# Kernel optimization log

Measured on AMD Instinct MI355X. Metric: run time of the kernel, lower is better.

## Reference

```python
import jax, jax.numpy as jnp
import numpy as np

V, H, E, L = 50257, 2048, 1024, 4


def setup_inputs() -> dict:
    key = jax.random.key(0)
    ks = jax.random.split(key, 9)
    s = 0.02
    emb = jax.random.normal(ks[0], (V, E), dtype=jnp.float32) * s
    W_ih0 = jax.random.normal(ks[1], (4 * H, E), dtype=jnp.float32) * s   # layer 0 input weights
    W_ihR = jax.random.normal(ks[2], (L - 1, 4 * H, H), dtype=jnp.float32) * s  # layers 1..L-1
    W_hh = jax.random.normal(ks[3], (L, 4 * H, H), dtype=jnp.float32) * s
    b_ih = jax.random.normal(ks[4], (L, 4 * H), dtype=jnp.float32) * s
    b_hh = jax.random.normal(ks[5], (L, 4 * H), dtype=jnp.float32) * s
    fc_W = jax.random.normal(ks[6], (E, H), dtype=jnp.float32) * s
    fc_b = jax.random.normal(ks[7], (E,), dtype=jnp.float32) * s
    inp = jax.random.randint(ks[8], (1,), 0, V, dtype=jnp.int64 if jax.config.jax_enable_x64 else jnp.int32)
    hidden = jnp.zeros((L, 1, H), dtype=jnp.float32)
    cell = jnp.zeros((L, 1, H), dtype=jnp.float32)
    return {"input": inp, "hidden": hidden, "cell": cell, "emb": emb,
            "W_ih0": W_ih0, "W_ihR": W_ihR, "W_hh": W_hh, "b_ih": b_ih,
            "b_hh": b_hh, "fc_W": fc_W, "fc_b": fc_b}


def reference(input, hidden, cell, emb, W_ih0, W_ihR, W_hh, b_ih, b_hh, fc_W, fc_b):
    # embedding lookup: [1, E]
    x = emb[input]
    h_out, c_out = [], []
    for l in range(L):  # small fixed layer loop (structurally distinct weights)
        W_ih = W_ih0 if l == 0 else W_ihR[l - 1]
        gates = x @ W_ih.T + hidden[l] @ W_hh[l].T + b_ih[l] + b_hh[l]  # [1, 4H]
        i, f, g, o = jnp.split(gates, 4, axis=-1)  # torch gate order i,f,g,o
        i, f, o = jax.nn.sigmoid(i), jax.nn.sigmoid(f), jax.nn.sigmoid(o)
        g = jnp.tanh(g)
        c = f * cell[l] + i * g
        h = o * jnp.tanh(c)
        h_out.append(h)
        c_out.append(c)
        x = h
    hidden_new = jnp.stack(h_out, axis=0)  # [L, 1, H]
    cell_new = jnp.stack(c_out, axis=0)
    decoded = x @ fc_W.T + fc_b  # [1, E]
    return decoded, hidden_new, cell_new
```

## Files before the change

kernel.cpp:

```cpp
#include <hip/hip_runtime.h>
#include <math.h>

#define LSTM_H 2048
#define LSTM_E 1024
#define LSTM_L 4

__device__ __forceinline__ float sigmoidf_(float x) {
    return 1.0f / (1.0f + __expf(-x));
}

template<int INW>
__global__ __launch_bounds__(256)
void lstm_layer_kernel(const float* __restrict__ W_ih,
                       const float* __restrict__ W_hh,
                       const float* __restrict__ b_ih,
                       const float* __restrict__ b_hh,
                       const float* __restrict__ xbase,
                       const int*   __restrict__ token,
                       const float* __restrict__ h_in,
                       const float* __restrict__ c_in,
                       float* __restrict__ h_out,
                       float* __restrict__ c_out)
{
    const int j    = blockIdx.x;
    const int wave = threadIdx.x >> 6;
    const int lane = threadIdx.x & 63;

    const float* x = xbase;
    if (token) x += (size_t)(*token) * (size_t)INW;

    const int row = wave * LSTM_H + j;

    const float4* __restrict__ wih4 = (const float4*)(W_ih + (size_t)row * INW);
    const float4* __restrict__ whh4 = (const float4*)(W_hh + (size_t)row * LSTM_H);
    const float4* __restrict__ x4   = (const float4*)x;
    const float4* __restrict__ h4   = (const float4*)h_in;

    float s = 0.0f;

    constexpr int NI = (INW / 4) / 64;
    #pragma unroll
    for (int t = 0; t < NI; ++t) {
        const int idx = lane + t * 64;
        float4 w = wih4[idx];
        float4 v = x4[idx];
        s += w.x * v.x + w.y * v.y + w.z * v.z + w.w * v.w;
    }

    constexpr int NH = (LSTM_H / 4) / 64;
    #pragma unroll
    for (int t = 0; t < NH; ++t) {
        const int idx = lane + t * 64;
        float4 w = whh4[idx];
        float4 v = h4[idx];
        s += w.x * v.x + w.y * v.y + w.z * v.z + w.w * v.w;
    }

    #pragma unroll
    for (int off = 32; off > 0; off >>= 1)
        s += __shfl_down(s, off, 64);

    __shared__ float gsh[4];
    if (lane == 0)
        gsh[wave] = s + b_ih[row] + b_hh[row];
    __syncthreads();

    if (threadIdx.x == 0) {
        const float gi = gsh[0];
        const float gf = gsh[1];
        const float gg = gsh[2];
        const float go = gsh[3];
        const float i_ = sigmoidf_(gi);
        const float f_ = sigmoidf_(gf);
        const float g_ = tanhf(gg);
        const float o_ = sigmoidf_(go);
        const float c  = f_ * c_in[j] + i_ * g_;
        const float h  = o_ * tanhf(c);
        c_out[j] = c;
        h_out[j] = h;
    }
}

__global__ __launch_bounds__(256)
void fc_kernel(const float* __restrict__ fc_W,
               const float* __restrict__ fc_b,
               const float* __restrict__ h,
               float* __restrict__ out)
{
    const int wave = threadIdx.x >> 6;
    const int lane = threadIdx.x & 63;
    const int r = blockIdx.x * 4 + wave;

    const float4* __restrict__ w4 = (const float4*)(fc_W + (size_t)r * LSTM_H);
    const float4* __restrict__ h4 = (const float4*)h;

    float s = 0.0f;
    constexpr int NH = (LSTM_H / 4) / 64;
    #pragma unroll
    for (int t = 0; t < NH; ++t) {
        const int idx = lane + t * 64;
        float4 w = w4[idx];
        float4 v = h4[idx];
        s += w.x * v.x + w.y * v.y + w.z * v.z + w.w * v.w;
    }

    #pragma unroll
    for (int off = 32; off > 0; off >>= 1)
        s += __shfl_down(s, off, 64);

    if (lane == 0)
        out[r] = s + fc_b[r];
}

extern "C" void kernel_launch(void* const* d_in, const int* in_sizes, int n_in,
                              void* d_out, int out_size, void* d_ws, size_t ws_size,
                              hipStream_t stream) {
    const int*   token  = (const int*)d_in[0];
    const float* hidden = (const float*)d_in[1];
    const float* cell   = (const float*)d_in[2];
    const float* emb    = (const float*)d_in[3];
    const float* W_ih0  = (const float*)d_in[4];
    const float* W_ihR  = (const float*)d_in[5];
    const float* W_hh   = (const float*)d_in[6];
    const float* b_ih   = (const float*)d_in[7];
    const float* b_hh   = (const float*)d_in[8];
    const float* fc_W   = (const float*)d_in[9];
    const float* fc_b   = (const float*)d_in[10];

    float* out     = (float*)d_out;
    float* decoded = out;
    float* h_new   = out + LSTM_E;
    float* c_new   = out + LSTM_E + LSTM_L * LSTM_H;

    const size_t WIH_STRIDE = (size_t)4 * LSTM_H * LSTM_H;
    const size_t B_STRIDE   = (size_t)4 * LSTM_H;

    lstm_layer_kernel<LSTM_E><<<LSTM_H, 256, 0, stream>>>(
        W_ih0, W_hh, b_ih, b_hh,
        emb, token,
        hidden, cell,
        h_new, c_new);

    for (int l = 1; l < LSTM_L; ++l) {
        lstm_layer_kernel<LSTM_H><<<LSTM_H, 256, 0, stream>>>(
            W_ihR + (size_t)(l - 1) * WIH_STRIDE,
            W_hh  + (size_t)l * WIH_STRIDE,
            b_ih  + (size_t)l * B_STRIDE,
            b_hh  + (size_t)l * B_STRIDE,
            h_new + (size_t)(l - 1) * LSTM_H, nullptr,
            hidden + (size_t)l * LSTM_H,
            cell   + (size_t)l * LSTM_H,
            h_new + (size_t)l * LSTM_H,
            c_new + (size_t)l * LSTM_H);
    }

    fc_kernel<<<LSTM_E / 4, 256, 0, stream>>>(
        fc_W, fc_b, h_new + (size_t)(LSTM_L - 1) * LSTM_H, decoded);
}
```

Before: 106.9 us.

## Fuse LSTM layers and FC into one cooperative kernel with early W_hh work

Replaces the five separate launches with one persistent cooperative kernel that uses grid-wide syncs between layers. The recurrent W_hh products for layers 1-3 depend only on the input hidden state, so they are computed up front and stored in workspace. This moves about half of the weight traffic off the serial layer-to-layer chain and removes launch gaps. The costs are grid.sync overhead, fewer resident blocks looping over rows, and reliance on the cooperative launch succeeding, with the old multi-kernel path kept as a fallback.

```diff
diff --git a/kernel.cpp b/kernel.cpp
--- a/kernel.cpp
+++ b/kernel.cpp
@@ -1,12 +1,151 @@
 #include <hip/hip_runtime.h>
+#include <hip/hip_cooperative_groups.h>
 #include <math.h>
 
 #define LSTM_H 2048
 #define LSTM_E 1024
 #define LSTM_L 4
 
+namespace cg = cooperative_groups;
+
 __device__ __forceinline__ float sigmoidf_(float x) {
     return 1.0f / (1.0f + __expf(-x));
+}
+
+__device__ __forceinline__ float wave_reduce(float s) {
+    #pragma unroll
+    for (int off = 32; off > 0; off >>= 1)
+        s += __shfl_down(s, off, 64);
+    return s;
+}
+
+__device__ __forceinline__ float dot2048(const float* __restrict__ w,
+                                         const float* __restrict__ v, int lane) {
+    const float4* __restrict__ w4 = (const float4*)w;
+    const float4* __restrict__ v4 = (const float4*)v;
+    float s = 0.0f;
+    #pragma unroll
+    for (int t = 0; t < 8; ++t) {
+        const int idx = lane + t * 64;
+        float4 a = w4[idx];
+        float4 b = v4[idx];
+        s += a.x * b.x + a.y * b.y + a.z * b.z + a.w * b.w;
+    }
+    return s;
+}
+
+__device__ __forceinline__ float dot1024(const float* __restrict__ w,
+                                         const float* __restrict__ v, int lane) {
+    const float4* __restrict__ w4 = (const float4*)w;
+    const float4* __restrict__ v4 = (const float4*)v;
+    float s = 0.0f;
+    #pragma unroll
+    for (int t = 0; t < 4; ++t) {
+        const int idx = lane + t * 64;
+        float4 a = w4[idx];
+        float4 b = v4[idx];
+        s += a.x * b.x + a.y * b.y + a.z * b.z + a.w * b.w;
+    }
+    return s;
+}
+
+__global__ __launch_bounds__(256, 4)
+void lstm_fused_kernel(const int*   __restrict__ token,
+                       const float* __restrict__ hidden,
+                       const float* __restrict__ cell,
+                       const float* __restrict__ emb,
+                       const float* __restrict__ W_ih0,
+                       const float* __restrict__ W_ihR,
+                       const float* __restrict__ W_hh,
+                       const float* __restrict__ b_ih,
+                       const float* __restrict__ b_hh,
+                       const float* __restrict__ fc_W,
+                       const float* __restrict__ fc_b,
+                       float*       __restrict__ out,
+                       float*       __restrict__ part)
+{
+    cg::grid_group grid = cg::this_grid();
+
+    const int G    = gridDim.x;
+    const int b    = blockIdx.x;
+    const int wave = threadIdx.x >> 6;
+    const int lane = threadIdx.x & 63;
+
+    float* decoded = out;
+    float* h_new   = out + LSTM_E;
+    float* c_new   = out + LSTM_E + LSTM_L * LSTM_H;
+
+    __shared__ float gsh[4];
+
+    const float* xemb = emb + (size_t)(*token) * LSTM_E;
+
+    for (int j = b; j < LSTM_H; j += G) {
+        const int row = wave * LSTM_H + j;
+        float s = dot1024(W_ih0 + (size_t)row * LSTM_E, xemb, lane)
+                + dot2048(W_hh  + (size_t)row * LSTM_H, hidden, lane);
+        s = wave_reduce(s);
+        if (lane == 0) gsh[wave] = s + b_ih[row] + b_hh[row];
+        __syncthreads();
+        if (threadIdx.x == 0) {
+            const float i_ = sigmoidf_(gsh[0]);
+            const float f_ = sigmoidf_(gsh[1]);
+            const float g_ = tanhf(gsh[2]);
+            const float o_ = sigmoidf_(gsh[3]);
+            const float c  = f_ * cell[j] + i_ * g_;
+            c_new[j] = c;
+            h_new[j] = o_ * tanhf(c);
+        }
+        __syncthreads();
+    }
+
+    #pragma unroll
+    for (int l = 1; l < LSTM_L; ++l) {
+        const float* hl = hidden + (size_t)l * LSTM_H;
+        for (int j = b; j < LSTM_H; j += G) {
+            const int row = wave * LSTM_H + j;
+            const size_t w_off = (size_t)l * 4 * LSTM_H * LSTM_H + (size_t)row * LSTM_H;
+            float s = dot2048(W_hh + w_off, hl, lane);
+            s = wave_reduce(s);
+            if (lane == 0)
+                part[(size_t)(l - 1) * 4 * LSTM_H + row] =
+                    s + b_ih[(size_t)l * 4 * LSTM_H + row]
+                      + b_hh[(size_t)l * 4 * LSTM_H + row];
+        }
+    }
+
+    grid.sync();
+
+    for (int l = 1; l < LSTM_L; ++l) {
+        const float* hx = h_new + (size_t)(l - 1) * LSTM_H;
+        for (int j = b; j < LSTM_H; j += G) {
+            const int row = wave * LSTM_H + j;
+            float s = dot2048(W_ihR + (size_t)(l - 1) * 4 * LSTM_H * LSTM_H
+                                    + (size_t)row * LSTM_H, hx, lane);
+            s = wave_reduce(s);
+            if (lane == 0) gsh[wave] = s + part[(size_t)(l - 1) * 4 * LSTM_H + row];
+            __syncthreads();
+            if (threadIdx.x == 0) {
+                const float i_ = sigmoidf_(gsh[0]);
+                const float f_ = sigmoidf_(gsh[1]);
+                const float g_ = tanhf(gsh[2]);
+                const float o_ = sigmoidf_(gsh[3]);
+                const float c  = f_ * cell[(size_t)l * LSTM_H + j] + i_ * g_;
+                c_new[(size_t)l * LSTM_H + j] = c;
+                h_new[(size_t)l * LSTM_H + j] = o_ * tanhf(c);
+            }
+            __syncthreads();
+        }
+        grid.sync();
+    }
+
+    {
+        const float* h3 = h_new + (size_t)(LSTM_L - 1) * LSTM_H;
+        for (int r = b * 4 + wave; r < LSTM_E; r += G * 4) {
+            float s = dot2048(fc_W + (size_t)r * LSTM_H, h3, lane);
+            s = wave_reduce(s);
+            if (lane == 0) decoded[r] = s + fc_b[r];
+        }
+    }
 }
 
 template<int INW>
@@ -31,53 +170,26 @@
 
     const int row = wave * LSTM_H + j;
 
-    const float4* __restrict__ wih4 = (const float4*)(W_ih + (size_t)row * INW);
-    const float4* __restrict__ whh4 = (const float4*)(W_hh + (size_t)row * LSTM_H);
-    const float4* __restrict__ x4   = (const float4*)x;
-    const float4* __restrict__ h4   = (const float4*)h_in;
-
     float s = 0.0f;
-
-    constexpr int NI = (INW / 4) / 64;
-    #pragma unroll
-    for (int t = 0; t < NI; ++t) {
-        const int idx = lane + t * 64;
-        float4 w = wih4[idx];
-        float4 v = x4[idx];
-        s += w.x * v.x + w.y * v.y + w.z * v.z + w.w * v.w;
-    }
-
-    constexpr int NH = (LSTM_H / 4) / 64;
-    #pragma unroll
-    for (int t = 0; t < NH; ++t) {
-        const int idx = lane + t * 64;
-        float4 w = whh4[idx];
-        float4 v = h4[idx];
-        s += w.x * v.x + w.y * v.y + w.z * v.z + w.w * v.w;
-    }
-
-    #pragma unroll
-    for (int off = 32; off > 0; off >>= 1)
-        s += __shfl_down(s, off, 64);
+    if (INW == LSTM_E)
+        s += dot1024(W_ih + (size_t)row * INW, x, lane);
+    else
+        s += dot2048(W_ih + (size_t)row * INW, x, lane);
+    s += dot2048(W_hh + (size_t)row * LSTM_H, h_in, lane);
+    s = wave_reduce(s);
 
     __shared__ float gsh[4];
-    if (lane == 0)
-        gsh[wave] = s + b_ih[row] + b_hh[row];
+    if (lane == 0) gsh[wave] = s + b_ih[row] + b_hh[row];
     __syncthreads();
 
     if (threadIdx.x == 0) {
-        const float gi = gsh[0];
-        const float gf = gsh[1];
-        const float gg = gsh[2];
-        const float go = gsh[3];
-        const float i_ = sigmoidf_(gi);
-        const float f_ = sigmoidf_(gf);
-        const float g_ = tanhf(gg);
-        const float o_ = sigmoidf_(go);
+        const float i_ = sigmoidf_(gsh[0]);
+        const float f_ = sigmoidf_(gsh[1]);
+        const float g_ = tanhf(gsh[2]);
+        const float o_ = sigmoidf_(gsh[3]);
         const float c  = f_ * c_in[j] + i_ * g_;
-        const float h  = o_ * tanhf(c);
         c_out[j] = c;
-        h_out[j] = h;
+        h_out[j] = o_ * tanhf(c);
     }
 }
 
@@ -91,25 +203,9 @@
     const int lane = threadIdx.x & 63;
     const int r = blockIdx.x * 4 + wave;
 
-    const float4* __restrict__ w4 = (const float4*)(fc_W + (size_t)r * LSTM_H);
-    const float4* __restrict__ h4 = (const float4*)h;
-
-    float s = 0.0f;
-    constexpr int NH = (LSTM_H / 4) / 64;
-    #pragma unroll
-    for (int t = 0; t < NH; ++t) {
-        const int idx = lane + t * 64;
-        float4 w = w4[idx];
-        float4 v = h4[idx];
-        s += w.x * v.x + w.y * v.y + w.z * v.z + w.w * v.w;
-    }
-
-    #pragma unroll
-    for (int off = 32; off > 0; off >>= 1)
-        s += __shfl_down(s, off, 64);
-
-    if (lane == 0)
-        out[r] = s + fc_b[r];
+    float s = dot2048(fc_W + (size_t)r * LSTM_H, h, lane);
+    s = wave_reduce(s);
+    if (lane == 0) out[r] = s + fc_b[r];
 }
 
 extern "C" void kernel_launch(void* const* d_in, const int* in_sizes, int n_in,
@@ -127,33 +223,64 @@
     const float* fc_W   = (const float*)d_in[9];
     const float* fc_b   = (const float*)d_in[10];
 
-    float* out     = (float*)d_out;
-    float* decoded = out;
-    float* h_new   = out + LSTM_E;
-    float* c_new   = out + LSTM_E + LSTM_L * LSTM_H;
-
-    const size_t WIH_STRIDE = (size_t)4 * LSTM_H * LSTM_H;
-    const size_t B_STRIDE   = (size_t)4 * LSTM_H;
-
-    lstm_layer_kernel<LSTM_E><<<LSTM_H, 256, 0, stream>>>(
-        W_ih0, W_hh, b_ih, b_hh,
-        emb, token,
-        hidden, cell,
-        h_new, c_new);
-
-    for (int l = 1; l < LSTM_L; ++l) {
-        lstm_layer_kernel<LSTM_H><<<LSTM_H, 256, 0, stream>>>(
-            W_ihR + (size_t)(l - 1) * WIH_STRIDE,
-            W_hh  + (size_t)l * WIH_STRIDE,
-            b_ih  + (size_t)l * B_STRIDE,
-            b_hh  + (size_t)l * B_STRIDE,
-            h_new + (size_t)(l - 1) * LSTM_H, nullptr,
-            hidden + (size_t)l * LSTM_H,
-            cell   + (size_t)l * LSTM_H,
-            h_new + (size_t)l * LSTM_H,
-            c_new + (size_t)l * LSTM_H);
-    }
-
-    fc_kernel<<<LSTM_E / 4, 256, 0, stream>>>(
-        fc_W, fc_b, h_new + (size_t)(LSTM_L - 1) * LSTM_H, decoded);
-}
+    float* out  = (float*)d_out;
+    float* part = (float*)d_ws;
+
+    void* args[] = {
+        (void*)&token, (void*)&hidden, (void*)&cell, (void*)&emb,
+        (void*)&W_ih0, (void*)&W_ihR, (void*)&W_hh, (void*)&b_ih,
+        (void*)&b_hh, (void*)&fc_W, (void*)&fc_b, (void*)&out, (void*)&part
+    };
+
+    int dev = 0;
+    (void)hipGetDevice(&dev);
+    int numCU = 256;
+    (void)hipDeviceGetAttribute(&numCU, hipDeviceAttributeMultiprocessorCount, dev);
+    int maxB = 0;
+    (void)hipOccupancyMaxActiveBlocksPerMultiprocessor(&maxB, lstm_fused_kernel, 256, 0);
+    if (maxB < 1) maxB = 1;
+
+    long cap = (long)numCU * (long)maxB;
+    int tries[3];
+    tries[0] = (int)(cap < 1024 ? cap : 1024);
+    tries[1] = 512;
+    tries[2] = 256;
+
+    hipError_t e = hipErrorUnknown;
+    int prev = 1 << 30;
+    for (int t = 0; t < 3; ++t) {
+        if (tries[t] >= prev || tries[t] < 1) continue;
+        prev = tries[t];
+        e = hipLaunchCooperativeKernel((void*)lstm_fused_kernel,
+                                       dim3(tries[t]), dim3(256), args, 0, stream);
+        if (e == hipSuccess) break;
+        (void)hipGetLastError();
+    }
+
+    if (e != hipSuccess) {
+        float* decoded = out;
+        float* h_new   = out + LSTM_E;
+        float* c_new   = out + LSTM_E + LSTM_L * LSTM_H;
+        const size_t WIH_STRIDE = (size_t)4 * LSTM_H * LSTM_H;
+        const size_t B_STRIDE   = (size_t)4 * LSTM_H;
+
+        lstm_layer_kernel<LSTM_E><<<LSTM_H, 256, 0, stream>>>(
+            W_ih0, W_hh, b_ih, b_hh, emb, token, hidden, cell, h_new, c_new);
+
+        for (int l = 1; l < LSTM_L; ++l) {
+            lstm_layer_kernel<LSTM_H><<<LSTM_H, 256, 0, stream>>>(
+                W_ihR + (size_t)(l - 1) * WIH_STRIDE,
+                W_hh  + (size_t)l * WIH_STRIDE,
+                b_ih  + (size_t)l * B_STRIDE,
+                b_hh  + (size_t)l * B_STRIDE,
+                h_new + (size_t)(l - 1) * LSTM_H, nullptr,
+                hidden + (size_t)l * LSTM_H,
+                cell   + (size_t)l * LSTM_H,
+                h_new + (size_t)l * LSTM_H,
+                c_new + (size_t)l * LSTM_H);
+        }
+
+        fc_kernel<<<LSTM_E / 4, 256, 0, stream>>>(
+            fc_W, fc_b, h_new + (size_t)(LSTM_L - 1) * LSTM_H, decoded);
+    }
+}
```

Result: slower. 362.9 us (+239.4%).

## Precompute all layers' recurrent W_hh partials in the first kernel

Applied to the files above, without the earlier changes.

Moves the hidden-state matvecs (W_hh·h_prev plus biases) for all four layers into the first kernel, because they do not depend on the previous layer's output. Their partial gate sums go to workspace, and layers 1-3 then read only W_ih. This gives the first kernel much more independent memory traffic, which should saturate bandwidth better. The dependent chain becomes shorter, at the cost of a heavier first launch and an extra workspace round trip.

```diff
diff --git a/kernel.cpp b/kernel.cpp
--- a/kernel.cpp
+++ b/kernel.cpp
@@ -9,107 +9,165 @@
     return 1.0f / (1.0f + __expf(-x));
 }
 
-template<int INW>
+__device__ __forceinline__ float wave_reduce(float s) {
+    #pragma unroll
+    for (int off = 32; off > 0; off >>= 1)
+        s += __shfl_down(s, off, 64);
+    return s;
+}
+
+__device__ __forceinline__ float dot2048(const float* __restrict__ w,
+                                         const float* __restrict__ v, int lane) {
+    const float4* __restrict__ w4 = (const float4*)w;
+    const float4* __restrict__ v4 = (const float4*)v;
+    float s = 0.0f;
+    #pragma unroll
+    for (int t = 0; t < 8; ++t) {
+        const int idx = lane + t * 64;
+        float4 a = w4[idx];
+        float4 b = v4[idx];
+        s += a.x * b.x + a.y * b.y + a.z * b.z + a.w * b.w;
+    }
+    return s;
+}
+
 __global__ __launch_bounds__(256)
-void lstm_layer_kernel(const float* __restrict__ W_ih,
+void k0_fused_partials(const int*   __restrict__ token,
+                       const float* __restrict__ hidden,
+                       const float* __restrict__ cell,
+                       const float* __restrict__ emb,
+                       const float* __restrict__ W_ih0,
                        const float* __restrict__ W_hh,
                        const float* __restrict__ b_ih,
                        const float* __restrict__ b_hh,
-                       const float* __restrict__ xbase,
-                       const int*   __restrict__ token,
-                       const float* __restrict__ h_in,
-                       const float* __restrict__ c_in,
-                       float* __restrict__ h_out,
-                       float* __restrict__ c_out)
+                       float* __restrict__ h_new,
+                       float* __restrict__ c_new,
+                       float* __restrict__ part)
 {
     const int j    = blockIdx.x;
     const int wave = threadIdx.x >> 6;
     const int lane = threadIdx.x & 63;
-
-    const float* x = xbase;
-    if (token) x += (size_t)(*token) * (size_t)INW;
-
-    const int row = wave * LSTM_H + j;
-
-    const float4* __restrict__ wih4 = (const float4*)(W_ih + (size_t)row * INW);
-    const float4* __restrict__ whh4 = (const float4*)(W_hh + (size_t)row * LSTM_H);
-    const float4* __restrict__ x4   = (const float4*)x;
-    const float4* __restrict__ h4   = (const float4*)h_in;
-
-    float s = 0.0f;
-
-    constexpr int NI = (INW / 4) / 64;
+    const int row  = wave * LSTM_H + j;
+
+    const float bias0 = b_ih[row] + b_hh[row];
+    const float bias1 = b_ih[1 * 4 * LSTM_H + row] + b_hh[1 * 4 * LSTM_H + row];
+    const float bias2 = b_ih[2 * 4 * LSTM_H + row] + b_hh[2 * 4 * LSTM_H + row];
+    const float bias3 = b_ih[3 * 4 * LSTM_H + row] + b_hh[3 * 4 * LSTM_H + row];
+    const float c_in0 = cell[j];
+
+    const float4* __restrict__ x4  = (const float4*)(emb + (size_t)(*token) * LSTM_E);
+    const float4* __restrict__ v0  = (const float4*)(hidden);
+    const float4* __restrict__ v1  = (const float4*)(hidden + LSTM_H);
+    const float4* __restrict__ v2  = (const float4*)(hidden + 2 * LSTM_H);
+    const float4* __restrict__ v3  = (const float4*)(hidden + 3 * LSTM_H);
+
+    const size_t LSTRIDE4 = (size_t)4 * LSTM_H * LSTM_H / 4;
+    const float4* __restrict__ w0 = (const float4*)(W_hh) + (size_t)row * (LSTM_H / 4);
+    const float4* __restrict__ w1 = w0 + LSTRIDE4;
+    const float4* __restrict__ w2 = w1 + LSTRIDE4;
+    const float4* __restrict__ w3 = w2 + LSTRIDE4;
+    const float4* __restrict__ wi = (const float4*)(W_ih0) + (size_t)row * (LSTM_E / 4);
+
+    float a0 = 0.f, a1 = 0.f, a2 = 0.f, a3 = 0.f, ax = 0.f;
+
     #pragma unroll
-    for (int t = 0; t < NI; ++t) {
+    for (int t = 0; t < 8; ++t) {
         const int idx = lane + t * 64;
-        float4 w = wih4[idx];
-        float4 v = x4[idx];
-        s += w.x * v.x + w.y * v.y + w.z * v.z + w.w * v.w;
-    }
-
-    constexpr int NH = (LSTM_H / 4) / 64;
-    #pragma unroll
-    for (int t = 0; t < NH; ++t) {
-        const int idx = lane + t * 64;
-        float4 w = whh4[idx];
-        float4 v = h4[idx];
-        s += w.x * v.x + w.y * v.y + w.z * v.z + w.w * v.w;
-    }
-
-    #pragma unroll
-    for (int off = 32; off > 0; off >>= 1)
-        s += __shfl_down(s, off, 64);
+        {
+            float4 w = w0[idx], v = v0[idx];
+            a0 += w.x * v.x + w.y * v.y + w.z * v.z + w.w * v.w;
+        }
+        {
+            float4 w = w1[idx], v = v1[idx];
+            a1 += w.x * v.x + w.y * v.y + w.z * v.z + w.w * v.w;
+        }
+        {
+            float4 w = w2[idx], v = v2[idx];
+            a2 += w.x * v.x + w.y * v.y + w.z * v.z + w.w * v.w;
+        }
+        {
+            float4 w = w3[idx], v = v3[idx];
+            a3 += w.x * v.x + w.y * v.y + w.z * v.z + w.w * v.w;
+        }
+        if (t < 4) {
+            float4 w = wi[idx], v = x4[idx];
+            ax += w.x * v.x + w.y * v.y + w.z * v.z + w.w * v.w;
+        }
+    }
+
+    const float g0 = wave_reduce(ax + a0);
+    const float p1 = wave_reduce(a1);
+    const float p2 = wave_reduce(a2);
+    const float p3 = wave_reduce(a3);
 
     __shared__ float gsh[4];
-    if (lane == 0)
-        gsh[wave] = s + b_ih[row] + b_hh[row];
+    if (lane == 0) {
+        gsh[wave] = g0 + bias0;
+        part[0 * 4 * LSTM_H + row] = p1 + bias1;
+        part[1 * 4 * LSTM_H + row] = p2 + bias2;
+        part[2 * 4 * LSTM_H + row] = p3 + bias3;
+    }
     __syncthreads();
 
     if (threadIdx.x == 0) {
-        const float gi = gsh[0];
-        const float gf = gsh[1];
-        const float gg = gsh[2];
-        const float go = gsh[3];
-        const float i_ = sigmoidf_(gi);
-        const float f_ = sigmoidf_(gf);
-        const float g_ = tanhf(gg);
-        const float o_ = sigmoidf_(go);
-        const float c  = f_ * c_in[j] + i_ * g_;
-        const float h  = o_ * tanhf(c);
+        const float i_ = sigmoidf_(gsh[0]);
+        const float f_ = sigmoidf_(gsh[1]);
+        const float g_ = tanhf(gsh[2]);
+        const float o_ = sigmoidf_(gsh[3]);
+        const float c  = f_ * c_in0 + i_ * g_;
+        c_new[j] = c;
+        h_new[j] = o_ * tanhf(c);
+    }
+}
+
+__global__ __launch_bounds__(256)
+void kb_layer(const float* __restrict__ W_ih,
+              const float* __restrict__ part_l,
+              const float* __restrict__ hx,
+              const float* __restrict__ c_in,
+              float* __restrict__ h_out,
+              float* __restrict__ c_out)
+{
+    const int j    = blockIdx.x;
+    const int wave = threadIdx.x >> 6;
+    const int lane = threadIdx.x & 63;
+    const int row  = wave * LSTM_H + j;
+
+    const float p    = part_l[row];
+    const float c_in_j = c_in[j];
+
+    float s = dot2048(W_ih + (size_t)row * LSTM_H, hx, lane);
+    s = wave_reduce(s);
+
+    __shared__ float gsh[4];
+    if (lane == 0) gsh[wave] = s + p;
+    __syncthreads();
+
+    if (threadIdx.x == 0) {
+        const float i_ = sigmoidf_(gsh[0]);
+        const float f_ = sigmoidf_(gsh[1]);
+        const float g_ = tanhf(gsh[2]);
+        const float o_ = sigmoidf_(gsh[3]);
+        const float c  = f_ * c_in_j + i_ * g_;
         c_out[j] = c;
-        h_out[j] = h;
+        h_out[j] = o_ * tanhf(c);
     }
 }
 
 __global__ __launch_bounds__(256)
-void fc_kernel(const float* __restrict__ fc_W,
-               const float* __restrict__ fc_b,
-               const float* __restrict__ h,
-               float* __restrict__ out)
+void kfc(const float* __restrict__ fc_W,
+         const float* __restrict__ fc_b,
+         const float* __restrict__ h,
+         float* __restrict__ out)
 {
     const int wave = threadIdx.x >> 6;
     const int lane = threadIdx.x & 63;
     const int r = blockIdx.x * 4 + wave;
 
-    const float4* __restrict__ w4 = (const float4*)(fc_W + (size_t)r * LSTM_H);
-    const float4* __restrict__ h4 = (const float4*)h;
-
-    float s = 0.0f;
-    constexpr int NH = (LSTM_H / 4) / 64;
-    #pragma unroll
-    for (int t = 0; t < NH; ++t) {
-        const int idx = lane + t * 64;
-        float4 w = w4[idx];
-        float4 v = h4[idx];
-        s += w.x * v.x + w.y * v.y + w.z * v.z + w.w * v.w;
-    }
-
-    #pragma unroll
-    for (int off = 32; off > 0; off >>= 1)
-        s += __shfl_down(s, off, 64);
-
-    if (lane == 0)
-        out[r] = s + fc_b[r];
+    const float b = fc_b[r];
+    float s = dot2048(fc_W + (size_t)r * LSTM_H, h, lane);
+    s = wave_reduce(s);
+    if (lane == 0) out[r] = s + b;
 }
 
 extern "C" void kernel_launch(void* const* d_in, const int* in_sizes, int n_in,
@@ -131,29 +189,25 @@
     float* decoded = out;
     float* h_new   = out + LSTM_E;
     float* c_new   = out + LSTM_E + LSTM_L * LSTM_H;
+    float* part    = (float*)d_ws;
 
     const size_t WIH_STRIDE = (size_t)4 * LSTM_H * LSTM_H;
-    const size_t B_STRIDE   = (size_t)4 * LSTM_H;
-
-    lstm_layer_kernel<LSTM_E><<<LSTM_H, 256, 0, stream>>>(
-        W_ih0, W_hh, b_ih, b_hh,
-        emb, token,
-        hidden, cell,
-        h_new, c_new);
+    const size_t P_STRIDE   = (size_t)4 * LSTM_H;
+
+    k0_fused_partials<<<LSTM_H, 256, 0, stream>>>(
+        token, hidden, cell, emb, W_ih0, W_hh, b_ih, b_hh,
+        h_new, c_new, part);
 
     for (int l = 1; l < LSTM_L; ++l) {
-        lstm_layer_kernel<LSTM_H><<<LSTM_H, 256, 0, stream>>>(
+        kb_layer<<<LSTM_H, 256, 0, stream>>>(
             W_ihR + (size_t)(l - 1) * WIH_STRIDE,
-            W_hh  + (size_t)l * WIH_STRIDE,
-            b_ih  + (size_t)l * B_STRIDE,
-            b_hh  + (size_t)l * B_STRIDE,
-            h_new + (size_t)(l - 1) * LSTM_H, nullptr,
-            hidden + (size_t)l * LSTM_H,
-            cell   + (size_t)l * LSTM_H,
+            part  + (size_t)(l - 1) * P_STRIDE,
+            h_new + (size_t)(l - 1) * LSTM_H,
+            cell  + (size_t)l * LSTM_H,
             h_new + (size_t)l * LSTM_H,
             c_new + (size_t)l * LSTM_H);
     }
 
-    fc_kernel<<<LSTM_E / 4, 256, 0, stream>>>(
+    kfc<<<LSTM_E / 4, 256, 0, stream>>>(
         fc_W, fc_b, h_new + (size_t)(LSTM_L - 1) * LSTM_H, decoded);
 }
```

Result: slower. 128.2 us (+19.9%).

## Hoist all recurrent matvecs into one upfront kernel and fuse gate activations downstream

Applied to the files above, without the earlier changes.

All W_hh·h_prev matvecs across layers, plus the layer-0 input projection, are moved into one large kernel, since they do not depend on the layer chain. Each later kernel first recomputes the previous layer's gate nonlinearities for all 2048 units into LDS, then does only the W_ih matvec. The last kernel fuses the final-layer activations with the FC projection. This takes the serial critical path from one 2x-sized matvec per layer to one per layer of half the work, with better parallelism up front. The cost is redundant activation work in every block and extra workspace round trips for gate values.

```diff
diff --git a/kernel.cpp b/kernel.cpp
--- a/kernel.cpp
+++ b/kernel.cpp
@@ -4,112 +4,188 @@
 #define LSTM_H 2048
 #define LSTM_E 1024
 #define LSTM_L 4
+#define FOURH  8192
 
 __device__ __forceinline__ float sigmoidf_(float x) {
     return 1.0f / (1.0f + __expf(-x));
 }
 
-template<int INW>
+__device__ __forceinline__ float wave_reduce(float s) {
+    #pragma unroll
+    for (int off = 32; off > 0; off >>= 1)
+        s += __shfl_down(s, off, 64);
+    return s;
+}
+
 __global__ __launch_bounds__(256)
-void lstm_layer_kernel(const float* __restrict__ W_ih,
-                       const float* __restrict__ W_hh,
-                       const float* __restrict__ b_ih,
-                       const float* __restrict__ b_hh,
-                       const float* __restrict__ xbase,
-                       const int*   __restrict__ token,
-                       const float* __restrict__ h_in,
-                       const float* __restrict__ c_in,
-                       float* __restrict__ h_out,
-                       float* __restrict__ c_out)
+void k1_rows(const int*   __restrict__ token,
+             const float* __restrict__ hidden,
+             const float* __restrict__ emb,
+             const float* __restrict__ W_ih0,
+             const float* __restrict__ W_hh,
+             const float* __restrict__ b_ih,
+             const float* __restrict__ b_hh,
+             float* __restrict__ A,
+             float* __restrict__ B,
+             float* __restrict__ part)
 {
-    const int j    = blockIdx.x;
     const int wave = threadIdx.x >> 6;
     const int lane = threadIdx.x & 63;
 
-    const float* x = xbase;
-    if (token) x += (size_t)(*token) * (size_t)INW;
-
-    const int row = wave * LSTM_H + j;
-
-    const float4* __restrict__ wih4 = (const float4*)(W_ih + (size_t)row * INW);
-    const float4* __restrict__ whh4 = (const float4*)(W_hh + (size_t)row * LSTM_H);
-    const float4* __restrict__ x4   = (const float4*)x;
-    const float4* __restrict__ h4   = (const float4*)h_in;
-
-    float s = 0.0f;
-
-    constexpr int NI = (INW / 4) / 64;
-    #pragma unroll
-    for (int t = 0; t < NI; ++t) {
-        const int idx = lane + t * 64;
-        float4 w = wih4[idx];
-        float4 v = x4[idx];
-        s += w.x * v.x + w.y * v.y + w.z * v.z + w.w * v.w;
-    }
-
-    constexpr int NH = (LSTM_H / 4) / 64;
-    #pragma unroll
-    for (int t = 0; t < NH; ++t) {
-        const int idx = lane + t * 64;
-        float4 w = whh4[idx];
-        float4 v = h4[idx];
-        s += w.x * v.x + w.y * v.y + w.z * v.z + w.w * v.w;
-    }
-
-    #pragma unroll
-    for (int off = 32; off > 0; off >>= 1)
-        s += __shfl_down(s, off, 64);
-
-    __shared__ float gsh[4];
-    if (lane == 0)
-        gsh[wave] = s + b_ih[row] + b_hh[row];
-    __syncthreads();
-
-    if (threadIdx.x == 0) {
-        const float gi = gsh[0];
-        const float gf = gsh[1];
-        const float gg = gsh[2];
-        const float go = gsh[3];
+    if (blockIdx.x < 2048) {
+        const int r = blockIdx.x * 4 + wave;
+        const float4* w4 = (const float4*)(W_ih0 + (size_t)r * LSTM_E);
+        const float4* v4 = (const float4*)(emb + (size_t)(*token) * LSTM_E);
+        float s = 0.f;
+        #pragma unroll
+        for (int t = 0; t < 4; ++t) {
+            const int idx = lane + t * 64;
+            float4 a = w4[idx], b = v4[idx];
+            s += a.x * b.x + a.y * b.y + a.z * b.z + a.w * b.w;
+        }
+        s = wave_reduce(s);
+        if (lane == 0) A[r] = s + b_ih[r] + b_hh[r];
+    } else {
+        const int R     = (blockIdx.x - 2048) * 4 + wave;
+        const int layer = R >> 13;
+        const int rowin = R & (FOURH - 1);
+        const float4* w4 = (const float4*)(W_hh + (size_t)layer * FOURH * LSTM_H
+                                                 + (size_t)rowin * LSTM_H);
+        const float4* v4 = (const float4*)(hidden + (size_t)layer * LSTM_H);
+        float s = 0.f;
+        #pragma unroll
+        for (int t = 0; t < 8; ++t) {
+            const int idx = lane + t * 64;
+            float4 a = w4[idx], b = v4[idx];
+            s += a.x * b.x + a.y * b.y + a.z * b.z + a.w * b.w;
+        }
+        s = wave_reduce(s);
+        if (lane == 0) {
+            if (layer == 0) B[rowin] = s;
+            else {
+                const size_t br = (size_t)layer * FOURH + rowin;
+                part[(size_t)(layer - 1) * FOURH + rowin] = s + b_ih[br] + b_hh[br];
+            }
+        }
+    }
+}
+
+__global__ __launch_bounds__(256)
+void kb_rows(const float* __restrict__ W,
+             const float* __restrict__ partl,
+             const float* __restrict__ gA,
+             const float* __restrict__ gB,
+             const float* __restrict__ c_in,
+             float* __restrict__ h_out_g,
+             float* __restrict__ c_out_g,
+             float* __restrict__ gates_out)
+{
+    __shared__ __align__(16) float h_lds[LSTM_H];
+    __shared__ __align__(16) float c_lds[LSTM_H];
+
+    const int t    = threadIdx.x;
+    const int wave = t >> 6;
+    const int lane = t & 63;
+    const int r    = blockIdx.x * 4 + wave;
+
+    const float4* __restrict__ w4 = (const float4*)(W + (size_t)r * LSTM_H);
+    float4 wreg[8];
+    #pragma unroll
+    for (int i = 0; i < 8; ++i) wreg[i] = w4[lane + i * 64];
+
+    const float p = partl[r];
+
+    #pragma unroll
+    for (int u = 0; u < 8; ++u) {
+        const int j = t + 256 * u;
+        float gi, gf, gg, go;
+        if (gB) {
+            gi = gA[j]          + gB[j];
+            gf = gA[j + 2048]   + gB[j + 2048];
+            gg = gA[j + 4096]   + gB[j + 4096];
+            go = gA[j + 6144]   + gB[j + 6144];
+        } else {
+            gi = gA[j]; gf = gA[j + 2048]; gg = gA[j + 4096]; go = gA[j + 6144];
+        }
         const float i_ = sigmoidf_(gi);
         const float f_ = sigmoidf_(gf);
         const float g_ = tanhf(gg);
         const float o_ = sigmoidf_(go);
         const float c  = f_ * c_in[j] + i_ * g_;
-        const float h  = o_ * tanhf(c);
-        c_out[j] = c;
-        h_out[j] = h;
-    }
+        c_lds[j] = c;
+        h_lds[j] = o_ * tanhf(c);
+    }
+    __syncthreads();
+
+    if (blockIdx.x < 256 && t < 8) {
+        const int j = blockIdx.x * 8 + t;
+        h_out_g[j] = h_lds[j];
+        c_out_g[j] = c_lds[j];
+    }
+
+    const float4* __restrict__ h4 = (const float4*)h_lds;
+    float s = 0.f;
+    #pragma unroll
+    for (int i = 0; i < 8; ++i) {
+        float4 v = h4[lane + i * 64];
+        s += wreg[i].x * v.x + wreg[i].y * v.y + wreg[i].z * v.z + wreg[i].w * v.w;
+    }
+    s = wave_reduce(s);
+    if (lane == 0) gates_out[r] = s + p;
 }
 
 __global__ __launch_bounds__(256)
-void fc_kernel(const float* __restrict__ fc_W,
-               const float* __restrict__ fc_b,
-               const float* __restrict__ h,
-               float* __restrict__ out)
+void kfc_rows(const float* __restrict__ fc_W,
+              const float* __restrict__ fc_b,
+              const float* __restrict__ g3,
+              const float* __restrict__ c_in,
+              float* __restrict__ h_out_g,
+              float* __restrict__ c_out_g,
+              float* __restrict__ decoded)
 {
-    const int wave = threadIdx.x >> 6;
-    const int lane = threadIdx.x & 63;
-    const int r = blockIdx.x * 4 + wave;
+    __shared__ __align__(16) float h_lds[LSTM_H];
+    __shared__ __align__(16) float c_lds[LSTM_H];
+
+    const int t    = threadIdx.x;
+    const int wave = t >> 6;
+    const int lane = t & 63;
+    const int r    = blockIdx.x * 4 + wave;
 
     const float4* __restrict__ w4 = (const float4*)(fc_W + (size_t)r * LSTM_H);
-    const float4* __restrict__ h4 = (const float4*)h;
-
-    float s = 0.0f;
-    constexpr int NH = (LSTM_H / 4) / 64;
-    #pragma unroll
-    for (int t = 0; t < NH; ++t) {
-        const int idx = lane + t * 64;
-        float4 w = w4[idx];
-        float4 v = h4[idx];
-        s += w.x * v.x + w.y * v.y + w.z * v.z + w.w * v.w;
-    }
-
-    #pragma unroll
-    for (int off = 32; off > 0; off >>= 1)
-        s += __shfl_down(s, off, 64);
-
-    if (lane == 0)
-        out[r] = s + fc_b[r];
+    float4 wreg[8];
+    #pragma unroll
+    for (int i = 0; i < 8; ++i) wreg[i] = w4[lane + i * 64];
+
+    const float fb = fc_b[r];
+
+    #pragma unroll
+    for (int u = 0; u < 8; ++u) {
+        const int j = t + 256 * u;
+        const float i_ = sigmoidf_(g3[j]);
+        const float f_ = sigmoidf_(g3[j + 2048]);
+        const float g_ = tanhf(g3[j + 4096]);
+        const float o_ = sigmoidf_(g3[j + 6144]);
+        const float c  = f_ * c_in[j] + i_ * g_;
+        c_lds[j] = c;
+        h_lds[j] = o_ * tanhf(c);
+    }
+    __syncthreads();
+
+    if (t < 8) {
+        const int j = blockIdx.x * 8 + t;
+        h_out_g[j] = h_lds[j];
+        c_out_g[j] = c_lds[j];
+    }
+
+    const float4* __restrict__ h4 = (const float4*)h_lds;
+    float s = 0.f;
+    #pragma unroll
+    for (int i = 0; i < 8; ++i) {
+        float4 v = h4[lane + i * 64];
+        s += wreg[i].x * v.x + wreg[i].y * v.y + wreg[i].z * v.z + wreg[i].w * v.w;
+    }
+    s = wave_reduce(s);
+    if (lane == 0) decoded[r] = s + fb;
 }
 
 extern "C" void kernel_launch(void* const* d_in, const int* in_sizes, int n_in,
@@ -132,28 +208,30 @@
     float* h_new   = out + LSTM_E;
     float* c_new   = out + LSTM_E + LSTM_L * LSTM_H;
 
-    const size_t WIH_STRIDE = (size_t)4 * LSTM_H * LSTM_H;
-    const size_t B_STRIDE   = (size_t)4 * LSTM_H;
-
-    lstm_layer_kernel<LSTM_E><<<LSTM_H, 256, 0, stream>>>(
-        W_ih0, W_hh, b_ih, b_hh,
-        emb, token,
-        hidden, cell,
-        h_new, c_new);
-
-    for (int l = 1; l < LSTM_L; ++l) {
-        lstm_layer_kernel<LSTM_H><<<LSTM_H, 256, 0, stream>>>(
-            W_ihR + (size_t)(l - 1) * WIH_STRIDE,
-            W_hh  + (size_t)l * WIH_STRIDE,
-            b_ih  + (size_t)l * B_STRIDE,
-            b_hh  + (size_t)l * B_STRIDE,
-            h_new + (size_t)(l - 1) * LSTM_H, nullptr,
-            hidden + (size_t)l * LSTM_H,
-            cell   + (size_t)l * LSTM_H,
-            h_new + (size_t)l * LSTM_H,
-            c_new + (size_t)l * LSTM_H);
-    }
-
-    fc_kernel<<<LSTM_E / 4, 256, 0, stream>>>(
-        fc_W, fc_b, h_new + (size_t)(LSTM_L - 1) * LSTM_H, decoded);
-}
+    float* ws    = (float*)d_ws;
+    float* A     = ws;
+    float* B     = ws + FOURH;
+    float* part  = ws + 2 * FOURH;
+    float* gates = ws + 5 * FOURH;
+
+    const size_t WIH_STRIDE = (size_t)FOURH * LSTM_H;
+
+    k1_rows<<<10240, 256, 0, stream>>>(
+        token, hidden, emb, W_ih0, W_hh, b_ih, b_hh, A, B, part);
+
+    kb_rows<<<2048, 256, 0, stream>>>(
+        W_ihR, part, A, B,
+        cell, h_new, c_new, gates);
+
+    kb_rows<<<2048, 256, 0, stream>>>(
+        W_ihR + WIH_STRIDE, part + FOURH, gates, nullptr,
+        cell + LSTM_H, h_new + LSTM_H, c_new + LSTM_H, gates + FOURH);
+
+    kb_rows<<<2048, 256, 0, stream>>>(
+        W_ihR + 2 * WIH_STRIDE, part + 2 * FOURH, gates + FOURH, nullptr,
+        cell + 2 * LSTM_H, h_new + 2 * LSTM_H, c_new + 2 * LSTM_H, gates + 2 * FOURH);
+
+    kfc_rows<<<LSTM_E / 4, 256, 0, stream>>>(
+        fc_W, fc_b, gates + 2 * FOURH,
+        cell + 3 * LSTM_H, h_new + 3 * LSTM_H, c_new + 3 * LSTM_H, decoded);
+}
```

New measurement: 123.2 us. 1.15x slower.
